# Performance work log

Measured on AMD Instinct MI355X. Metric: run time of the kernel, lower is better.

Reference implementation:

```python
import jax, jax.numpy as jnp
import numpy as np

N = 512      # N_res
C = 128      # act_dim == num_intermediate_channel
EPS = 1e-5   # torch LayerNorm default


def _layernorm(x, w, b):
    mu = jnp.mean(x, axis=-1, keepdims=True)
    var = jnp.var(x, axis=-1, keepdims=True)
    return (x - mu) * jax.lax.rsqrt(var + EPS) * w + b


def setup_inputs() -> dict:
    key = jax.random.key(0)
    ks = jax.random.split(key, 12)
    s_in = 1.0 / np.sqrt(C)
    inp = {
        "act": jax.random.normal(ks[0], (N, N, C), dtype=jnp.float32),
        "mask": jax.random.uniform(ks[1], (N, N), dtype=jnp.float32),
        # left_norm_input (LayerNorm over act_dim)
        "ln_in_w": jnp.ones((C,), jnp.float32),
        "ln_in_b": jnp.zeros((C,), jnp.float32),
        # projection: Linear(C -> 2C)
        "proj_w": jax.random.uniform(ks[2], (2 * C, C), jnp.float32, -s_in, s_in),
        "proj_b": jax.random.uniform(ks[3], (2 * C,), jnp.float32, -s_in, s_in),
        # gate: Linear(C -> 2C)
        "gate_w": jax.random.uniform(ks[4], (2 * C, C), jnp.float32, -s_in, s_in),
        "gate_b": jax.random.uniform(ks[5], (2 * C,), jnp.float32, -s_in, s_in),
        # center_norm (LayerNorm over num_intermediate_channel)
        "cn_w": jnp.ones((C,), jnp.float32),
        "cn_b": jnp.zeros((C,), jnp.float32),
        # output_projection: Linear(C -> C)
        "outp_w": jax.random.uniform(ks[6], (C, C), jnp.float32, -s_in, s_in),
        "outp_b": jax.random.uniform(ks[7], (C,), jnp.float32, -s_in, s_in),
        # gating_linear: Linear(C -> C)
        "gl_w": jax.random.uniform(ks[8], (C, C), jnp.float32, -s_in, s_in),
        "gl_b": jax.random.uniform(ks[9], (C,), jnp.float32, -s_in, s_in),
    }
    return inp


def reference(act, mask, ln_in_w, ln_in_b, proj_w, proj_b, gate_w, gate_b,
              cn_w, cn_b, outp_w, outp_b, gl_w, gl_b):
    m = mask[..., None]                                  # [N,N,1]
    x = _layernorm(act, ln_in_w, ln_in_b)                # [N,N,C]
    input_act = x
    proj = m * (jnp.einsum('ijc,dc->ijd', x, proj_w) + proj_b)      # [N,N,2C]
    proj = proj * jax.nn.sigmoid(jnp.einsum('ijc,dc->ijd', x, gate_w) + gate_b)
    left, right = proj[..., :C], proj[..., C:]           # each [N,N,C]
    # outgoing-edges triangular multiplication
    out = jnp.einsum('ikc,jkc->ijc', left, right)        # [N,N,C]
    out = _layernorm(out, cn_w, cn_b)
    out = jnp.einsum('ijc,dc->ijd', out, outp_w) + outp_b
    out = out * jax.nn.sigmoid(jnp.einsum('ijc,dc->ijd', input_act, gl_w) + gl_b)
    return out
```

## Files before the change

### kernel.cpp

```cpp
#include <hip/hip_runtime.h>
#include <hip/hip_bf16.h>


constexpr int TN = 512;
constexpr int TC = 128;
constexpr int TNP = TN * TN;
constexpr float TEPS = 1e-5f;

typedef __attribute__((ext_vector_type(8))) short s8b;
typedef __attribute__((ext_vector_type(4))) float f4;

__device__ __forceinline__ float wredsum(float v) {
#pragma unroll
    for (int off = 32; off > 0; off >>= 1) v += __shfl_xor(v, off);
    return v;
}
__device__ __forceinline__ float sigmoidf(float x) { return 1.0f / (1.0f + __expf(-x)); }
__device__ __forceinline__ unsigned short bfbits(float f) {
    __hip_bfloat16 h = __float2bfloat16(f);
    return *reinterpret_cast<unsigned short*>(&h);
}
__device__ __forceinline__ float bf2f(unsigned short u) {
    return __uint_as_float(((unsigned int)u) << 16);
}


extern "C" __global__ __launch_bounds__(256)
void k_wconv(const float* __restrict__ pw, const float* __restrict__ gw,
             const float* __restrict__ ow, const float* __restrict__ glw,
             const float* __restrict__ cnw,
             __hip_bfloat16* __restrict__ warr, __hip_bfloat16* __restrict__ wcat2)
{
    const int idx = blockIdx.x * 256 + threadIdx.x;
    if (idx < 65536) {
        const int j = idx & 7;
        const int slot = (idx >> 3) & 63;
        const int kg = (idx >> 9) & 3;
        const int rg = (idx >> 11) & 7;
        const int nc = idx >> 14;
        const int lh = slot & 15, lq = slot >> 4;
        const int row = rg * 16 + lh;
        const int k = kg * 32 + lq * 8 + j;
        const float v = (row < 64) ? pw[(nc * 64 + row) * TC + k]
                                   : gw[(nc * 64 + (row - 64)) * TC + k];
        warr[idx] = __float2bfloat16(v);
    } else if (idx < 98304) {
        const int j = idx - 65536;
        if (j < 16384) {
            const int c = j & 127;
            wcat2[j] = __float2bfloat16(cnw[c] * ow[j]);
        } else {
            wcat2[j] = __float2bfloat16(glw[j - 16384]);
        }
    }
}

extern "C" __global__ __launch_bounds__(128)
void k_sdt(const float* __restrict__ ow, const float* __restrict__ cnw,
           const float* __restrict__ cnb, const float* __restrict__ outp_b,
           float* __restrict__ Svec, float* __restrict__ Tbvec)
{
    const int d = threadIdx.x;
    float S = 0.f, T = 0.f;
    for (int c = 0; c < TC; ++c) {
        const float w = ow[d * TC + c];
        S += cnw[c] * w;
        T += cnb[c] * w;
    }
    Svec[d] = S;
    Tbvec[d] = T + outp_b[d];
}

extern "C" __global__ __launch_bounds__(256)
void k_ln(const float* __restrict__ act, const float* __restrict__ lnw,
          const float* __restrict__ lnb, __hip_bfloat16* __restrict__ xhp)
{
    __shared__ __align__(16) unsigned short t16[16 * 136];
    const int t = threadIdx.x, lane = t & 63, w = t >> 6;
    const int P0 = blockIdx.x * 64;
    const float2 wv = ((const float2*)lnw)[lane];
    const float2 bv = ((const float2*)lnb)[lane];
    unsigned short* xb = (unsigned short*)xhp;

    for (int r = 0; r < 4; ++r) {
#pragma unroll
        for (int q = 0; q < 4; ++q) {
            const int prow = w * 4 + q;
            const int p = P0 + r * 16 + prow;
            const float2 a = ((const float2*)(act + (size_t)p * TC))[lane];
            const float mu = wredsum(a.x + a.y) * (1.0f / 128.0f);
            const float d0 = a.x - mu, d1 = a.y - mu;
            const float var = wredsum(d0 * d0 + d1 * d1) * (1.0f / 128.0f);
            const float rs = rsqrtf(var + TEPS);
            ushort2 o;
            o.x = bfbits(d0 * rs * wv.x + bv.x);
            o.y = bfbits(d1 * rs * wv.y + bv.y);
            *(ushort2*)&t16[prow * 136 + lane * 2] = o;
        }
        __syncthreads();
        {
            const int kg = t >> 6, lq = (t >> 4) & 3, lh = t & 15;
            const s8b v = *(const s8b*)&t16[lh * 136 + kg * 32 + lq * 8];
            *(s8b*)(xb + (size_t)((P0 >> 4) + r) * 2048 + (size_t)t * 8) = v;
        }
        __syncthreads();
    }
}

extern "C" __global__ __launch_bounds__(256)
void k_proj(const __hip_bfloat16* __restrict__ xhp, const float* __restrict__ mask,
            const __hip_bfloat16* __restrict__ warr,
            const float* __restrict__ proj_b, const float* __restrict__ gate_b,
            __hip_bfloat16* __restrict__ lt, __hip_bfloat16* __restrict__ rt)
{
    __shared__ __align__(16) unsigned short Xls[128 * TC];
    __shared__ float msk[128];
    unsigned short* tls = Xls;

    const int t = threadIdx.x, lane = t & 63, w = t >> 6;
    const int lh = lane & 15, lq = lane >> 4;

    const int bid = blockIdx.x;
    const int work = (bid & 7) * 1024 + (bid >> 3);
    const int pt = work >> 2, dt = work & 3;
    const int P0 = pt * 128;

    const unsigned short* xb = (const unsigned short*)xhp;
    const unsigned short* wbc = (const unsigned short*)warr + (size_t)dt * 16384;

    if (t < 128) msk[t] = mask[P0 + t];

    const int wm = w >> 1, wn = w & 1;

#pragma unroll
    for (int s = 0; s < 8; ++s) {
        const int u = w * 8 + s;
        const size_t gu = ((size_t)(P0 >> 4) + (u >> 2)) * 4 + (u & 3);
        __builtin_amdgcn_global_load_lds(
            (const __attribute__((address_space(1))) unsigned*)(xb + gu * 512 + (size_t)lane * 8),
            (__attribute__((address_space(3))) unsigned*)&Xls[u * 512], 16, 0, 0);
    }

    s8b bc[4], bn[4];
#pragma unroll
    for (int nd = 0; nd < 2; ++nd) {
        bc[nd]     = *(const s8b*)(wbc + (size_t)(((wn * 2 + nd) * 4) + 0) * 512 + lane * 8);
        bc[2 + nd] = *(const s8b*)(wbc + (size_t)(((4 + wn * 2 + nd) * 4) + 0) * 512 + lane * 8);
    }
    __syncthreads();

    f4 acc[4][4];
#pragma unroll
    for (int mi = 0; mi < 4; ++mi)
#pragma unroll
        for (int ni = 0; ni < 4; ++ni)
            acc[mi][ni] = (f4){0.f, 0.f, 0.f, 0.f};

#pragma unroll
    for (int kg = 0; kg < 4; ++kg) {
        if (kg < 3) {
#pragma unroll
            for (int nd = 0; nd < 2; ++nd) {
                bn[nd]     = *(const s8b*)(wbc + (size_t)(((wn * 2 + nd) * 4) + kg + 1) * 512 + lane * 8);
                bn[2 + nd] = *(const s8b*)(wbc + (size_t)(((4 + wn * 2 + nd) * 4) + kg + 1) * 512 + lane * 8);
            }
        }
        s8b af[4];
#pragma unroll
        for (int mi = 0; mi < 4; ++mi)
            af[mi] = *(const s8b*)&Xls[(((wm * 4 + mi) * 4) + kg) * 512 + lane * 8];
#pragma unroll
        for (int mi = 0; mi < 4; ++mi)
#pragma unroll
            for (int ni = 0; ni < 4; ++ni)
                acc[mi][ni] = __builtin_amdgcn_mfma_f32_16x16x32_bf16(
                    af[mi], bc[ni], acc[mi][ni], 0, 0, 0);
        if (kg < 3) {
#pragma unroll
            for (int ni = 0; ni < 4; ++ni) bc[ni] = bn[ni];
        }
    }
    __syncthreads();

#pragma unroll
    for (int mi = 0; mi < 4; ++mi)
#pragma unroll
        for (int nd = 0; nd < 2; ++nd) {
            const int dl = wn * 32 + nd * 16 + lh;
            const float pbv = proj_b[dt * 64 + dl];
            const float gbv = gate_b[dt * 64 + dl];
            const f4 P = acc[mi][nd];
            const f4 G = acc[mi][2 + nd];
            const int pbase = wm * 64 + mi * 16 + lq * 4;
            float v[4];
#pragma unroll
            for (int r = 0; r < 4; ++r)
                v[r] = msk[pbase + r] * (P[r] + pbv) * sigmoidf(G[r] + gbv);
            ushort2 u01, u23;
            u01.x = bfbits(v[0]); u01.y = bfbits(v[1]);
            u23.x = bfbits(v[2]); u23.y = bfbits(v[3]);
            *(ushort2*)&tls[dl * 134 + pbase]     = u01;
            *(ushort2*)&tls[dl * 134 + pbase + 2] = u23;
        }
    __syncthreads();

    {
        __hip_bfloat16* dst0 = (dt < 2) ? lt + (size_t)(dt * 64) * TNP
                                        : rt + (size_t)((dt - 2) * 64) * TNP;
#pragma unroll
        for (int rr = 0; rr < 16; ++rr) {
            const int dl = w * 16 + rr;
            const ushort2 v = *(const ushort2*)&tls[dl * 134 + lane * 2];
            *(ushort2*)((unsigned short*)(dst0 + (size_t)dl * TNP) + P0 + lane * 2) = v;
        }
    }
}

extern "C" __global__ __launch_bounds__(256)
void k_tri_mfma(const __hip_bfloat16* __restrict__ lt,
                const __hip_bfloat16* __restrict__ rt,
                __hip_bfloat16* __restrict__ trih)
{
    __shared__ __align__(16) char smem[128 * 136 * 2];
    __hip_bfloat16* Als = (__hip_bfloat16*)smem;
    __hip_bfloat16* Bls = (__hip_bfloat16*)(smem + 8192);
    unsigned short* Cls = (unsigned short*)smem;

    const int bid = blockIdx.x;
    const int work = (bid & 7) * 256 + (bid >> 3);
    const int c = work >> 4, tt = work & 15;
    const int i0 = (tt >> 2) * 128, j0 = (tt & 3) * 128;

    const int t = threadIdx.x;
    const int w = t >> 6, lane = t & 63;
    const int wm = w >> 1, wn = w & 1;
    const int lh = lane & 15, lq = lane >> 4;

    const size_t cbase = (size_t)c * TNP;
    const int srow = lane >> 2;
    const int scol = (lane & 3) * 8;

    f4 acc[4][4];
#pragma unroll
    for (int mi = 0; mi < 4; ++mi)
#pragma unroll
        for (int ni = 0; ni < 4; ++ni)
            acc[mi][ni] = (f4){0.f, 0.f, 0.f, 0.f};

    for (int k0 = 0; k0 < TN; k0 += 32) {
        __syncthreads();
#pragma unroll
        for (int s = 0; s < 2; ++s) {
            const int r0 = w * 32 + s * 16;
            const __hip_bfloat16* ga = lt + cbase + (size_t)(i0 + r0 + srow) * TN + k0 + scol;
            const __hip_bfloat16* gb = rt + cbase + (size_t)(j0 + r0 + srow) * TN + k0 + scol;
            __builtin_amdgcn_global_load_lds(
                (const __attribute__((address_space(1))) unsigned*)ga,
                (__attribute__((address_space(3))) unsigned*)&Als[r0 * 32], 16, 0, 0);
            __builtin_amdgcn_global_load_lds(
                (const __attribute__((address_space(1))) unsigned*)gb,
                (__attribute__((address_space(3))) unsigned*)&Bls[r0 * 32], 16, 0, 0);
        }
        __syncthreads();

        s8b afr[4], bfr[4];
#pragma unroll
        for (int mi = 0; mi < 4; ++mi)
            afr[mi] = *(const s8b*)&Als[(wm * 64 + mi * 16 + lh) * 32 + lq * 8];
#pragma unroll
        for (int ni = 0; ni < 4; ++ni)
            bfr[ni] = *(const s8b*)&Bls[(wn * 64 + ni * 16 + lh) * 32 + lq * 8];
#pragma unroll
        for (int mi = 0; mi < 4; ++mi)
#pragma unroll
            for (int ni = 0; ni < 4; ++ni)
                acc[mi][ni] = __builtin_amdgcn_mfma_f32_16x16x32_bf16(
                    afr[mi], bfr[ni], acc[mi][ni], 0, 0, 0);
    }

    __syncthreads();
#pragma unroll
    for (int mi = 0; mi < 4; ++mi)
#pragma unroll
        for (int ni = 0; ni < 4; ++ni) {
            const f4 v = acc[mi][ni];
            const int jl = wn * 64 + ni * 16 + lh;
#pragma unroll
            for (int r = 0; r < 4; ++r) {
                const int il = wm * 64 + mi * 16 + lq * 4 + r;
                Cls[il * 136 + jl] = bfbits(v[r]);
            }
        }
    __syncthreads();
    {
        unsigned short* ob = (unsigned short*)trih + cbase;
#pragma unroll
        for (int qq = 0; qq < 8; ++qq) {
            const int row = qq * 16 + (t >> 4);
            const int c16 = t & 15;
            const s8b v = *(const s8b*)&Cls[row * 136 + c16 * 8];
            *(s8b*)&ob[(size_t)(i0 + row) * TN + j0 + c16 * 8] = v;
        }
    }
}

constexpr int PB = 64;

extern "C" __global__ __launch_bounds__(256)
void k_out_proj(const __hip_bfloat16* __restrict__ trih,
                const __hip_bfloat16* __restrict__ xhp,
                const __hip_bfloat16* __restrict__ wcat2,
                const float* __restrict__ Svec, const float* __restrict__ Tbvec,
                const float* __restrict__ gl_b,
                float* __restrict__ outb)
{
    __shared__ __align__(16) unsigned short yfr[PB * TC];
    __shared__ float2 sred[4][PB];
    __shared__ float2 stats[PB];

    const int t = threadIdx.x, lane = t & 63, w = t >> 6;
    const int lh = lane & 15, lq = lane >> 4;
    const int P0 = blockIdx.x * PB;
    const unsigned short* tb = (const unsigned short*)trih;
    const unsigned short* xb = (const unsigned short*)xhp;
    const unsigned short* wb = (const unsigned short*)wcat2;

    {
        const int p = lane;
        const int ub = (p >> 4) * 4 + w;
        const int sl = p & 15;
        float s = 0.f, s2 = 0.f;
#pragma unroll
        for (int q = 0; q < 4; ++q) {
            unsigned short tmp[8];
#pragma unroll
            for (int j = 0; j < 8; ++j) {
                const int c = w * 32 + q * 8 + j;
                tmp[j] = tb[(size_t)c * TNP + P0 + p];
                const float f = bf2f(tmp[j]);
                s += f; s2 += f * f;
            }
            *(s8b*)&yfr[ub * 512 + (q * 16 + sl) * 8] = *(const s8b*)tmp;
        }
        sred[w][p] = make_float2(s, s2);
    }
    __syncthreads();
    if (t < PB) {
        float s = 0.f, s2 = 0.f;
#pragma unroll
        for (int g = 0; g < 4; ++g) {
            const float2 v = sred[g][t];
            s += v.x; s2 += v.y;
        }
        const float mu = s * (1.0f / 128.0f);
        const float var = s2 * (1.0f / 128.0f) - mu * mu;
        stats[t] = make_float2(mu, rsqrtf(var + TEPS));
    }
    __syncthreads();

    const int dO = w * 32;
    const int dG = 128 + w * 32;

    f4 acc[4][4];
#pragma unroll
    for (int mi = 0; mi < 4; ++mi)
#pragma unroll
        for (int ni = 0; ni < 4; ++ni)
            acc[mi][ni] = (f4){0.f, 0.f, 0.f, 0.f};

#pragma unroll
    for (int kg = 0; kg < 4; ++kg) {
        s8b bo[2], bg[2], ay[4], ah[4];
#pragma unroll
        for (int nd = 0; nd < 2; ++nd) {
            bo[nd] = *(const s8b*)(wb + (dO + nd * 16 + lh) * TC + kg * 32 + lq * 8);
            bg[nd] = *(const s8b*)(wb + (dG + nd * 16 + lh) * TC + kg * 32 + lq * 8);
        }
#pragma unroll
        for (int mi = 0; mi < 4; ++mi) {
            ay[mi] = *(const s8b*)&yfr[(mi * 4 + kg) * 512 + lane * 8];
            ah[mi] = *(const s8b*)(xb + (size_t)((P0 >> 4) + mi) * 2048
                                      + kg * 512 + (size_t)lane * 8);
        }
#pragma unroll
        for (int mi = 0; mi < 4; ++mi)
#pragma unroll
            for (int nd = 0; nd < 2; ++nd) {
                acc[mi][nd]     = __builtin_amdgcn_mfma_f32_16x16x32_bf16(
                    ay[mi], bo[nd], acc[mi][nd], 0, 0, 0);
                acc[mi][2 + nd] = __builtin_amdgcn_mfma_f32_16x16x32_bf16(
                    ah[mi], bg[nd], acc[mi][2 + nd], 0, 0, 0);
            }
    }

    float Sd[2], Tbd[2], glb[2];
#pragma unroll
    for (int nd = 0; nd < 2; ++nd) {
        const int d = w * 32 + nd * 16 + lh;
        Sd[nd]  = Svec[d];
        Tbd[nd] = Tbvec[d];
        glb[nd] = gl_b[d];
    }
#pragma unroll
    for (int mi = 0; mi < 4; ++mi)
#pragma unroll
        for (int nd = 0; nd < 2; ++nd) {
            const f4 G = acc[mi][nd];
            const f4 Gg = acc[mi][2 + nd];
            const int d = w * 32 + nd * 16 + lh;
#pragma unroll
            for (int r = 0; r < 4; ++r) {
                const int ploc = mi * 16 + lq * 4 + r;
                const float2 st = stats[ploc];
                const float o = st.y * G[r] - st.y * st.x * Sd[nd] + Tbd[nd];
                outb[(size_t)(P0 + ploc) * TC + d] = o * sigmoidf(Gg[r] + glb[nd]);
            }
        }
}

extern "C" void kernel_launch(void* const* d_in, const int* in_sizes, int n_in,
                              void* d_out, int out_size, void* d_ws, size_t ws_size,
                              hipStream_t stream)
{
    const float* act    = (const float*)d_in[0];
    const float* mask   = (const float*)d_in[1];
    const float* lnw    = (const float*)d_in[2];
    const float* lnb    = (const float*)d_in[3];
    const float* proj_w = (const float*)d_in[4];
    const float* proj_b = (const float*)d_in[5];
    const float* gate_w = (const float*)d_in[6];
    const float* gate_b = (const float*)d_in[7];
    const float* cnw    = (const float*)d_in[8];
    const float* cnb    = (const float*)d_in[9];
    const float* outp_w = (const float*)d_in[10];
    const float* outp_b = (const float*)d_in[11];
    const float* gl_w   = (const float*)d_in[12];
    const float* gl_b   = (const float*)d_in[13];

    __hip_bfloat16* lt   = (__hip_bfloat16*)d_ws;
    __hip_bfloat16* rt   = lt + (size_t)TC * TNP;
    __hip_bfloat16* xhp  = rt + (size_t)TC * TNP;
    __hip_bfloat16* trih = xhp + (size_t)TNP * TC;
    __hip_bfloat16* warr = trih + (size_t)TC * TNP;
    __hip_bfloat16* wcat2 = warr + 4 * 128 * TC;
    float* Svec  = (float*)(wcat2 + 2 * TC * TC);
    float* Tbvec = Svec + TC;
    float* out = (float*)d_out;

    k_wconv<<<384, 256, 0, stream>>>(proj_w, gate_w, outp_w, gl_w, cnw, warr, wcat2);
    k_sdt<<<1, 128, 0, stream>>>(outp_w, cnw, cnb, outp_b, Svec, Tbvec);
    k_ln<<<TNP / 64, 256, 0, stream>>>(act, lnw, lnb, xhp);
    k_proj<<<8192, 256, 0, stream>>>(xhp, mask, warr, proj_b, gate_b, lt, rt);
    k_tri_mfma<<<2048, 256, 0, stream>>>(lt, rt, trih);
    k_out_proj<<<TNP / PB, 256, 0, stream>>>(trih, xhp, wcat2, Svec, Tbvec,
                                             gl_b, out);
}
```

Before: 282.2 us.

## Fuse gating-linear GEMM into projection kernel and store sigmoid gate as bf16

The gating_linear weights are packed into the projection weight array, so k_proj runs a fifth MFMA column tile per k-step and writes sigmoid(x·Wg + b) as a bf16 [N,N,C] buffer. k_out_proj then only runs the output-projection GEMM and multiplies by the loaded gate, no longer rereading the normalized input or doing the second GEMM. The triangular output buffer now aliases the no-longer-needed normalized-input buffer to keep the workspace small. In exchange, k_proj gains extra registers and accumulators and drops its weight prefetch double-buffering, the 32 MB gate tensor must be written and read back, and the gate is rounded to bf16.

```diff
diff --git a/kernel.cpp b/kernel.cpp
--- a/kernel.cpp
+++ b/kernel.cpp
@@ -32,26 +32,25 @@
              __hip_bfloat16* __restrict__ warr, __hip_bfloat16* __restrict__ wcat2)
 {
     const int idx = blockIdx.x * 256 + threadIdx.x;
-    if (idx < 65536) {
-        const int j = idx & 7;
-        const int slot = (idx >> 3) & 63;
-        const int kg = (idx >> 9) & 3;
-        const int rg = (idx >> 11) & 7;
-        const int nc = idx >> 14;
+    if (idx < 81920) {
+        const int nc = idx / 20480;
+        const int rem = idx % 20480;
+        const int unit = rem >> 9;
+        const int rg = unit >> 2, kg = unit & 3;
+        const int off = rem & 511;
+        const int slot = off >> 3, j = off & 7;
         const int lh = slot & 15, lq = slot >> 4;
         const int row = rg * 16 + lh;
         const int k = kg * 32 + lq * 8 + j;
-        const float v = (row < 64) ? pw[(nc * 64 + row) * TC + k]
-                                   : gw[(nc * 64 + (row - 64)) * TC + k];
+        float v;
+        if (row < 64)       v = pw[(nc * 64 + row) * TC + k];
+        else if (row < 128) v = gw[(nc * 64 + (row - 64)) * TC + k];
+        else                v = glw[(nc * 32 + (row - 128)) * TC + k];
         warr[idx] = __float2bfloat16(v);
-    } else if (idx < 98304) {
-        const int j = idx - 65536;
-        if (j < 16384) {
-            const int c = j & 127;
-            wcat2[j] = __float2bfloat16(cnw[c] * ow[j]);
-        } else {
-            wcat2[j] = __float2bfloat16(glw[j - 16384]);
-        }
+    } else {
+        const int j2 = idx - 81920;
+        const int c = j2 & 127;
+        wcat2[j2] = __float2bfloat16(cnw[c] * ow[j2]);
     }
 }
 
@@ -111,7 +110,9 @@
 void k_proj(const __hip_bfloat16* __restrict__ xhp, const float* __restrict__ mask,
             const __hip_bfloat16* __restrict__ warr,
             const float* __restrict__ proj_b, const float* __restrict__ gate_b,
-            __hip_bfloat16* __restrict__ lt, __hip_bfloat16* __restrict__ rt)
+            const float* __restrict__ gl_b,
+            __hip_bfloat16* __restrict__ lt, __hip_bfloat16* __restrict__ rt,
+            __hip_bfloat16* __restrict__ glgb)
 {
     __shared__ __align__(16) unsigned short Xls[128 * TC];
     __shared__ float msk[128];
@@ -126,7 +127,8 @@
     const int P0 = pt * 128;
 
     const unsigned short* xb = (const unsigned short*)xhp;
-    const unsigned short* wbc = (const unsigned short*)warr + (size_t)dt * 16384;
+    const unsigned short* wbc = (const unsigned short*)warr + (size_t)dt * 20480;
+    unsigned short* gb = (unsigned short*)glgb;
 
     if (t < 128) msk[t] = mask[P0 + t];
 
@@ -140,47 +142,48 @@
             (const __attribute__((address_space(1))) unsigned*)(xb + gu * 512 + (size_t)lane * 8),
             (__attribute__((address_space(3))) unsigned*)&Xls[u * 512], 16, 0, 0);
     }
-
-    s8b bc[4], bn[4];
-#pragma unroll
-    for (int nd = 0; nd < 2; ++nd) {
-        bc[nd]     = *(const s8b*)(wbc + (size_t)(((wn * 2 + nd) * 4) + 0) * 512 + lane * 8);
-        bc[2 + nd] = *(const s8b*)(wbc + (size_t)(((4 + wn * 2 + nd) * 4) + 0) * 512 + lane * 8);
-    }
-    __syncthreads();
-
-    f4 acc[4][4];
-#pragma unroll
-    for (int mi = 0; mi < 4; ++mi)
-#pragma unroll
-        for (int ni = 0; ni < 4; ++ni)
+    __syncthreads();
+
+    f4 acc[4][5];
+#pragma unroll
+    for (int mi = 0; mi < 4; ++mi)
+#pragma unroll
+        for (int ni = 0; ni < 5; ++ni)
             acc[mi][ni] = (f4){0.f, 0.f, 0.f, 0.f};
 
 #pragma unroll
     for (int kg = 0; kg < 4; ++kg) {
-        if (kg < 3) {
-#pragma unroll
-            for (int nd = 0; nd < 2; ++nd) {
-                bn[nd]     = *(const s8b*)(wbc + (size_t)(((wn * 2 + nd) * 4) + kg + 1) * 512 + lane * 8);
-                bn[2 + nd] = *(const s8b*)(wbc + (size_t)(((4 + wn * 2 + nd) * 4) + kg + 1) * 512 + lane * 8);
-            }
-        }
-        s8b af[4];
+        s8b bfr[5], af[4];
+#pragma unroll
+        for (int nd = 0; nd < 2; ++nd) {
+            bfr[nd]     = *(const s8b*)(wbc + (size_t)(((wn * 2 + nd) * 4) + kg) * 512 + lane * 8);
+            bfr[2 + nd] = *(const s8b*)(wbc + (size_t)((((4 + wn * 2 + nd)) * 4) + kg) * 512 + lane * 8);
+        }
+        bfr[4] = *(const s8b*)(wbc + (size_t)(((8 + wn) * 4) + kg) * 512 + lane * 8);
 #pragma unroll
         for (int mi = 0; mi < 4; ++mi)
             af[mi] = *(const s8b*)&Xls[(((wm * 4 + mi) * 4) + kg) * 512 + lane * 8];
 #pragma unroll
         for (int mi = 0; mi < 4; ++mi)
 #pragma unroll
-            for (int ni = 0; ni < 4; ++ni)
+            for (int ni = 0; ni < 5; ++ni)
                 acc[mi][ni] = __builtin_amdgcn_mfma_f32_16x16x32_bf16(
-                    af[mi], bc[ni], acc[mi][ni], 0, 0, 0);
-        if (kg < 3) {
-#pragma unroll
-            for (int ni = 0; ni < 4; ++ni) bc[ni] = bn[ni];
-        }
-    }
-    __syncthreads();
+                    af[mi], bfr[ni], acc[mi][ni], 0, 0, 0);
+    }
+    __syncthreads();
+
+    {
+        const float glbv = gl_b[dt * 32 + wn * 16 + lh];
+#pragma unroll
+        for (int mi = 0; mi < 4; ++mi) {
+            const f4 Gl = acc[mi][4];
+            const int pbase = wm * 64 + mi * 16 + lq * 4;
+#pragma unroll
+            for (int r = 0; r < 4; ++r)
+                gb[(size_t)(P0 + pbase + r) * TC + dt * 32 + wn * 16 + lh] =
+                    bfbits(sigmoidf(Gl[r] + glbv));
+        }
+    }
 
 #pragma unroll
     for (int mi = 0; mi < 4; ++mi)
@@ -253,12 +256,12 @@
         for (int s = 0; s < 2; ++s) {
             const int r0 = w * 32 + s * 16;
             const __hip_bfloat16* ga = lt + cbase + (size_t)(i0 + r0 + srow) * TN + k0 + scol;
-            const __hip_bfloat16* gb = rt + cbase + (size_t)(j0 + r0 + srow) * TN + k0 + scol;
+            const __hip_bfloat16* gbp = rt + cbase + (size_t)(j0 + r0 + srow) * TN + k0 + scol;
             __builtin_amdgcn_global_load_lds(
                 (const __attribute__((address_space(1))) unsigned*)ga,
                 (__attribute__((address_space(3))) unsigned*)&Als[r0 * 32], 16, 0, 0);
             __builtin_amdgcn_global_load_lds(
-                (const __attribute__((address_space(1))) unsigned*)gb,
+                (const __attribute__((address_space(1))) unsigned*)gbp,
                 (__attribute__((address_space(3))) unsigned*)&Bls[r0 * 32], 16, 0, 0);
         }
         __syncthreads();
@@ -308,10 +311,9 @@
 
 extern "C" __global__ __launch_bounds__(256)
 void k_out_proj(const __hip_bfloat16* __restrict__ trih,
-                const __hip_bfloat16* __restrict__ xhp,
+                const __hip_bfloat16* __restrict__ glgb,
                 const __hip_bfloat16* __restrict__ wcat2,
                 const float* __restrict__ Svec, const float* __restrict__ Tbvec,
-                const float* __restrict__ gl_b,
                 float* __restrict__ outb)
 {
     __shared__ __align__(16) unsigned short yfr[PB * TC];
@@ -322,7 +324,7 @@
     const int lh = lane & 15, lq = lane >> 4;
     const int P0 = blockIdx.x * PB;
     const unsigned short* tb = (const unsigned short*)trih;
-    const unsigned short* xb = (const unsigned short*)xhp;
+    const unsigned short* gb = (const unsigned short*)glgb;
     const unsigned short* wb = (const unsigned short*)wcat2;
 
     {
@@ -359,61 +361,51 @@
     __syncthreads();
 
     const int dO = w * 32;
-    const int dG = 128 + w * 32;
-
-    f4 acc[4][4];
-#pragma unroll
-    for (int mi = 0; mi < 4; ++mi)
-#pragma unroll
-        for (int ni = 0; ni < 4; ++ni)
+
+    f4 acc[4][2];
+#pragma unroll
+    for (int mi = 0; mi < 4; ++mi)
+#pragma unroll
+        for (int ni = 0; ni < 2; ++ni)
             acc[mi][ni] = (f4){0.f, 0.f, 0.f, 0.f};
 
 #pragma unroll
     for (int kg = 0; kg < 4; ++kg) {
-        s8b bo[2], bg[2], ay[4], ah[4];
-#pragma unroll
-        for (int nd = 0; nd < 2; ++nd) {
+        s8b bo[2], ay[4];
+#pragma unroll
+        for (int nd = 0; nd < 2; ++nd)
             bo[nd] = *(const s8b*)(wb + (dO + nd * 16 + lh) * TC + kg * 32 + lq * 8);
-            bg[nd] = *(const s8b*)(wb + (dG + nd * 16 + lh) * TC + kg * 32 + lq * 8);
-        }
-#pragma unroll
-        for (int mi = 0; mi < 4; ++mi) {
+#pragma unroll
+        for (int mi = 0; mi < 4; ++mi)
             ay[mi] = *(const s8b*)&yfr[(mi * 4 + kg) * 512 + lane * 8];
-            ah[mi] = *(const s8b*)(xb + (size_t)((P0 >> 4) + mi) * 2048
-                                      + kg * 512 + (size_t)lane * 8);
-        }
-#pragma unroll
-        for (int mi = 0; mi < 4; ++mi)
-#pragma unroll
-            for (int nd = 0; nd < 2; ++nd) {
-                acc[mi][nd]     = __builtin_amdgcn_mfma_f32_16x16x32_bf16(
+#pragma unroll
+        for (int mi = 0; mi < 4; ++mi)
+#pragma unroll
+            for (int nd = 0; nd < 2; ++nd)
+                acc[mi][nd] = __builtin_amdgcn_mfma_f32_16x16x32_bf16(
                     ay[mi], bo[nd], acc[mi][nd], 0, 0, 0);
-                acc[mi][2 + nd] = __builtin_amdgcn_mfma_f32_16x16x32_bf16(
-                    ah[mi], bg[nd], acc[mi][2 + nd], 0, 0, 0);
-            }
-    }
-
-    float Sd[2], Tbd[2], glb[2];
+    }
+
+    float Sd[2], Tbd[2];
 #pragma unroll
     for (int nd = 0; nd < 2; ++nd) {
         const int d = w * 32 + nd * 16 + lh;
         Sd[nd]  = Svec[d];
         Tbd[nd] = Tbvec[d];
-        glb[nd] = gl_b[d];
     }
 #pragma unroll
     for (int mi = 0; mi < 4; ++mi)
 #pragma unroll
         for (int nd = 0; nd < 2; ++nd) {
             const f4 G = acc[mi][nd];
-            const f4 Gg = acc[mi][2 + nd];
             const int d = w * 32 + nd * 16 + lh;
 #pragma unroll
             for (int r = 0; r < 4; ++r) {
                 const int ploc = mi * 16 + lq * 4 + r;
                 const float2 st = stats[ploc];
                 const float o = st.y * G[r] - st.y * st.x * Sd[nd] + Tbd[nd];
-                outb[(size_t)(P0 + ploc) * TC + d] = o * sigmoidf(Gg[r] + glb[nd]);
+                const float g = bf2f(gb[(size_t)(P0 + ploc) * TC + d]);
+                outb[(size_t)(P0 + ploc) * TC + d] = o * g;
             }
         }
 }
@@ -440,18 +432,19 @@
     __hip_bfloat16* lt   = (__hip_bfloat16*)d_ws;
     __hip_bfloat16* rt   = lt + (size_t)TC * TNP;
     __hip_bfloat16* xhp  = rt + (size_t)TC * TNP;
-    __hip_bfloat16* trih = xhp + (size_t)TNP * TC;
-    __hip_bfloat16* warr = trih + (size_t)TC * TNP;
-    __hip_bfloat16* wcat2 = warr + 4 * 128 * TC;
-    float* Svec  = (float*)(wcat2 + 2 * TC * TC);
+    __hip_bfloat16* trih = xhp;
+    __hip_bfloat16* glgb = xhp + (size_t)TNP * TC;
+    __hip_bfloat16* warr = glgb + (size_t)TNP * TC;
+    __hip_bfloat16* wcat2 = warr + 81920;
+    float* Svec  = (float*)(wcat2 + 16384);
     float* Tbvec = Svec + TC;
     float* out = (float*)d_out;
 
     k_wconv<<<384, 256, 0, stream>>>(proj_w, gate_w, outp_w, gl_w, cnw, warr, wcat2);
     k_sdt<<<1, 128, 0, stream>>>(outp_w, cnw, cnb, outp_b, Svec, Tbvec);
     k_ln<<<TNP / 64, 256, 0, stream>>>(act, lnw, lnb, xhp);
-    k_proj<<<8192, 256, 0, stream>>>(xhp, mask, warr, proj_b, gate_b, lt, rt);
+    k_proj<<<8192, 256, 0, stream>>>(xhp, mask, warr, proj_b, gate_b, gl_b,
+                                     lt, rt, glgb);
     k_tri_mfma<<<2048, 256, 0, stream>>>(lt, rt, trih);
-    k_out_proj<<<TNP / PB, 256, 0, stream>>>(trih, xhp, wcat2, Svec, Tbvec,
-                                             gl_b, out);
-}
+    k_out_proj<<<TNP / PB, 256, 0, stream>>>(trih, glgb, wcat2, Svec, Tbvec, out);
+}
```

Result: slower. 295.8 us (+4.8%).

## Restructure output projection into single-wave blocks over 16 positions and half the channels

Applied to the files above, without the earlier changes.

The output-projection kernel now runs one 64-thread wave per block, covering 16 positions and 64 output channels, instead of 256 threads covering 64 positions. LayerNorm statistics are reduced with wave shuffles instead of shared-memory reductions and block barriers. The goal is more, smaller blocks with no block-level syncs, for better latency hiding and occupancy. In exchange, each 16-position tile of the triangular-multiply output is read and normalised twice (once per channel half), and there are many more tiny blocks to schedule.

```diff
diff --git a/kernel.cpp b/kernel.cpp
--- a/kernel.cpp
+++ b/kernel.cpp
@@ -253,12 +253,12 @@
         for (int s = 0; s < 2; ++s) {
             const int r0 = w * 32 + s * 16;
             const __hip_bfloat16* ga = lt + cbase + (size_t)(i0 + r0 + srow) * TN + k0 + scol;
-            const __hip_bfloat16* gb = rt + cbase + (size_t)(j0 + r0 + srow) * TN + k0 + scol;
+            const __hip_bfloat16* gbp = rt + cbase + (size_t)(j0 + r0 + srow) * TN + k0 + scol;
             __builtin_amdgcn_global_load_lds(
                 (const __attribute__((address_space(1))) unsigned*)ga,
                 (__attribute__((address_space(3))) unsigned*)&Als[r0 * 32], 16, 0, 0);
             __builtin_amdgcn_global_load_lds(
-                (const __attribute__((address_space(1))) unsigned*)gb,
+                (const __attribute__((address_space(1))) unsigned*)gbp,
                 (__attribute__((address_space(3))) unsigned*)&Bls[r0 * 32], 16, 0, 0);
         }
         __syncthreads();
@@ -304,9 +304,7 @@
     }
 }
 
-constexpr int PB = 64;
-
-extern "C" __global__ __launch_bounds__(256)
+extern "C" __global__ __launch_bounds__(64)
 void k_out_proj(const __hip_bfloat16* __restrict__ trih,
                 const __hip_bfloat16* __restrict__ xhp,
                 const __hip_bfloat16* __restrict__ wcat2,
@@ -314,108 +312,77 @@
                 const float* __restrict__ gl_b,
                 float* __restrict__ outb)
 {
-    __shared__ __align__(16) unsigned short yfr[PB * TC];
-    __shared__ float2 sred[4][PB];
-    __shared__ float2 stats[PB];
-
-    const int t = threadIdx.x, lane = t & 63, w = t >> 6;
+    __shared__ __align__(16) unsigned short yfr[4 * 512];
+
+    const int lane = threadIdx.x;
     const int lh = lane & 15, lq = lane >> 4;
-    const int P0 = blockIdx.x * PB;
+    const int bid = blockIdx.x;
+    const int g = bid >> 1;
+    const int D0 = (bid & 1) * 64;
+    const int P0 = g * 16;
     const unsigned short* tb = (const unsigned short*)trih;
     const unsigned short* xb = (const unsigned short*)xhp;
     const unsigned short* wb = (const unsigned short*)wcat2;
 
-    {
-        const int p = lane;
-        const int ub = (p >> 4) * 4 + w;
-        const int sl = p & 15;
-        float s = 0.f, s2 = 0.f;
-#pragma unroll
-        for (int q = 0; q < 4; ++q) {
-            unsigned short tmp[8];
-#pragma unroll
-            for (int j = 0; j < 8; ++j) {
-                const int c = w * 32 + q * 8 + j;
-                tmp[j] = tb[(size_t)c * TNP + P0 + p];
-                const float f = bf2f(tmp[j]);
-                s += f; s2 += f * f;
-            }
-            *(s8b*)&yfr[ub * 512 + (q * 16 + sl) * 8] = *(const s8b*)tmp;
-        }
-        sred[w][p] = make_float2(s, s2);
-    }
-    __syncthreads();
-    if (t < PB) {
-        float s = 0.f, s2 = 0.f;
-#pragma unroll
-        for (int g = 0; g < 4; ++g) {
-            const float2 v = sred[g][t];
-            s += v.x; s2 += v.y;
-        }
-        const float mu = s * (1.0f / 128.0f);
-        const float var = s2 * (1.0f / 128.0f) - mu * mu;
-        stats[t] = make_float2(mu, rsqrtf(var + TEPS));
-    }
-    __syncthreads();
-
-    const int dO = w * 32;
-    const int dG = 128 + w * 32;
-
-    f4 acc[4][4];
-#pragma unroll
-    for (int mi = 0; mi < 4; ++mi)
-#pragma unroll
-        for (int ni = 0; ni < 4; ++ni)
-            acc[mi][ni] = (f4){0.f, 0.f, 0.f, 0.f};
-
+    float s = 0.f, s2 = 0.f;
 #pragma unroll
     for (int kg = 0; kg < 4; ++kg) {
-        s8b bo[2], bg[2], ay[4], ah[4];
-#pragma unroll
-        for (int nd = 0; nd < 2; ++nd) {
-            bo[nd] = *(const s8b*)(wb + (dO + nd * 16 + lh) * TC + kg * 32 + lq * 8);
-            bg[nd] = *(const s8b*)(wb + (dG + nd * 16 + lh) * TC + kg * 32 + lq * 8);
-        }
-#pragma unroll
-        for (int mi = 0; mi < 4; ++mi) {
-            ay[mi] = *(const s8b*)&yfr[(mi * 4 + kg) * 512 + lane * 8];
-            ah[mi] = *(const s8b*)(xb + (size_t)((P0 >> 4) + mi) * 2048
-                                      + kg * 512 + (size_t)lane * 8);
-        }
-#pragma unroll
-        for (int mi = 0; mi < 4; ++mi)
-#pragma unroll
-            for (int nd = 0; nd < 2; ++nd) {
-                acc[mi][nd]     = __builtin_amdgcn_mfma_f32_16x16x32_bf16(
-                    ay[mi], bo[nd], acc[mi][nd], 0, 0, 0);
-                acc[mi][2 + nd] = __builtin_amdgcn_mfma_f32_16x16x32_bf16(
-                    ah[mi], bg[nd], acc[mi][2 + nd], 0, 0, 0);
-            }
-    }
-
-    float Sd[2], Tbd[2], glb[2];
-#pragma unroll
-    for (int nd = 0; nd < 2; ++nd) {
-        const int d = w * 32 + nd * 16 + lh;
-        Sd[nd]  = Svec[d];
-        Tbd[nd] = Tbvec[d];
-        glb[nd] = gl_b[d];
-    }
-#pragma unroll
-    for (int mi = 0; mi < 4; ++mi)
-#pragma unroll
-        for (int nd = 0; nd < 2; ++nd) {
-            const f4 G = acc[mi][nd];
-            const f4 Gg = acc[mi][2 + nd];
-            const int d = w * 32 + nd * 16 + lh;
-#pragma unroll
-            for (int r = 0; r < 4; ++r) {
-                const int ploc = mi * 16 + lq * 4 + r;
-                const float2 st = stats[ploc];
-                const float o = st.y * G[r] - st.y * st.x * Sd[nd] + Tbd[nd];
-                outb[(size_t)(P0 + ploc) * TC + d] = o * sigmoidf(Gg[r] + glb[nd]);
-            }
-        }
+        unsigned short tmp[8];
+#pragma unroll
+        for (int j = 0; j < 8; ++j) {
+            const int c = kg * 32 + lq * 8 + j;
+            tmp[j] = tb[(size_t)c * TNP + P0 + lh];
+            const float f = bf2f(tmp[j]);
+            s += f; s2 += f * f;
+        }
+        *(s8b*)&yfr[kg * 512 + lane * 8] = *(const s8b*)tmp;
+    }
+    s  += __shfl_xor(s, 16);  s  += __shfl_xor(s, 32);
+    s2 += __shfl_xor(s2, 16); s2 += __shfl_xor(s2, 32);
+    const float mu = s * (1.0f / 128.0f);
+    const float var = s2 * (1.0f / 128.0f) - mu * mu;
+    const float rs = rsqrtf(var + TEPS);
+    __builtin_amdgcn_wave_barrier();
+
+    f4 acc[8];
+#pragma unroll
+    for (int i = 0; i < 8; ++i) acc[i] = (f4){0.f, 0.f, 0.f, 0.f};
+
+#pragma unroll
+    for (int kg = 0; kg < 4; ++kg) {
+        const s8b ay = *(const s8b*)&yfr[kg * 512 + lane * 8];
+        const s8b ah = *(const s8b*)(xb + (size_t)g * 2048 + kg * 512 + (size_t)lane * 8);
+#pragma unroll
+        for (int nd = 0; nd < 4; ++nd) {
+            const int d = D0 + nd * 16 + lh;
+            const s8b bo = *(const s8b*)(wb + (size_t)d * TC + kg * 32 + lq * 8);
+            const s8b bg = *(const s8b*)(wb + (size_t)(128 + d) * TC + kg * 32 + lq * 8);
+            acc[nd]     = __builtin_amdgcn_mfma_f32_16x16x32_bf16(ay, bo, acc[nd], 0, 0, 0);
+            acc[4 + nd] = __builtin_amdgcn_mfma_f32_16x16x32_bf16(ah, bg, acc[4 + nd], 0, 0, 0);
+        }
+    }
+
+    float mus[4], rss[4];
+#pragma unroll
+    for (int r = 0; r < 4; ++r) {
+        mus[r] = __shfl(mu, lq * 4 + r);
+        rss[r] = __shfl(rs, lq * 4 + r);
+    }
+
+#pragma unroll
+    for (int nd = 0; nd < 4; ++nd) {
+        const int d = D0 + nd * 16 + lh;
+        const float Sd  = Svec[d];
+        const float Tbd = Tbvec[d];
+        const float glb = gl_b[d];
+        const f4 G  = acc[nd];
+        const f4 Gl = acc[4 + nd];
+#pragma unroll
+        for (int r = 0; r < 4; ++r) {
+            const float o = rss[r] * G[r] - rss[r] * mus[r] * Sd + Tbd;
+            outb[(size_t)(P0 + lq * 4 + r) * TC + d] = o * sigmoidf(Gl[r] + glb);
+        }
+    }
 }
 
 extern "C" void kernel_launch(void* const* d_in, const int* in_sizes, int n_in,
@@ -452,6 +419,6 @@
     k_ln<<<TNP / 64, 256, 0, stream>>>(act, lnw, lnb, xhp);
     k_proj<<<8192, 256, 0, stream>>>(xhp, mask, warr, proj_b, gate_b, lt, rt);
     k_tri_mfma<<<2048, 256, 0, stream>>>(lt, rt, trih);
-    k_out_proj<<<TNP / PB, 256, 0, stream>>>(trih, xhp, wcat2, Svec, Tbvec,
-                                             gl_b, out);
-}
+    k_out_proj<<<TNP / 16 * 2, 64, 0, stream>>>(trih, xhp, wcat2, Svec, Tbvec,
+                                                gl_b, out);
+}
```

Result: slower. 364.3 us (+29.1%).

## Enlarge out-projection tile and stage output through LDS for coalesced stores

Applied to the files above, without the earlier changes.

The output-projection kernel now handles 128 positions per block with 512 threads instead of 64 positions with 256. Each thread reads two adjacent positions per channel as ushort2 when loading the channel-major triangle result. Work is split across a 4x2 wave grid. The final fp32 output is written into a reused LDS tile in two passes and then stored as float4 rows, replacing scattered scalar stores. This targets poor coalescing on both the transposed input reads and the output writes, at the cost of more LDS traffic and extra barriers.

```diff
diff --git a/kernel.cpp b/kernel.cpp
--- a/kernel.cpp
+++ b/kernel.cpp
@@ -253,12 +253,12 @@
         for (int s = 0; s < 2; ++s) {
             const int r0 = w * 32 + s * 16;
             const __hip_bfloat16* ga = lt + cbase + (size_t)(i0 + r0 + srow) * TN + k0 + scol;
-            const __hip_bfloat16* gb = rt + cbase + (size_t)(j0 + r0 + srow) * TN + k0 + scol;
+            const __hip_bfloat16* gbp = rt + cbase + (size_t)(j0 + r0 + srow) * TN + k0 + scol;
             __builtin_amdgcn_global_load_lds(
                 (const __attribute__((address_space(1))) unsigned*)ga,
                 (__attribute__((address_space(3))) unsigned*)&Als[r0 * 32], 16, 0, 0);
             __builtin_amdgcn_global_load_lds(
-                (const __attribute__((address_space(1))) unsigned*)gb,
+                (const __attribute__((address_space(1))) unsigned*)gbp,
                 (__attribute__((address_space(3))) unsigned*)&Bls[r0 * 32], 16, 0, 0);
         }
         __syncthreads();
@@ -304,9 +304,7 @@
     }
 }
 
-constexpr int PB = 64;
-
-extern "C" __global__ __launch_bounds__(256)
+extern "C" __global__ __launch_bounds__(512)
 void k_out_proj(const __hip_bfloat16* __restrict__ trih,
                 const __hip_bfloat16* __restrict__ xhp,
                 const __hip_bfloat16* __restrict__ wcat2,
@@ -314,42 +312,49 @@
                 const float* __restrict__ gl_b,
                 float* __restrict__ outb)
 {
-    __shared__ __align__(16) unsigned short yfr[PB * TC];
-    __shared__ float2 sred[4][PB];
-    __shared__ float2 stats[PB];
+    __shared__ __align__(16) char smem[41984];
+    unsigned short* yfr = (unsigned short*)smem;
+    float2* sred = (float2*)(smem + 32768);
+    float2* stats = (float2*)(smem + 40960);
+    float* otile = (float*)smem;
 
     const int t = threadIdx.x, lane = t & 63, w = t >> 6;
     const int lh = lane & 15, lq = lane >> 4;
-    const int P0 = blockIdx.x * PB;
+    const int P0 = blockIdx.x * 128;
     const unsigned short* tb = (const unsigned short*)trih;
     const unsigned short* xb = (const unsigned short*)xhp;
     const unsigned short* wb = (const unsigned short*)wcat2;
 
     {
-        const int p = lane;
-        const int ub = (p >> 4) * 4 + w;
-        const int sl = p & 15;
+        const int p0 = 2 * lane, p1 = 2 * lane + 1;
+        float s0 = 0.f, s20 = 0.f, s1 = 0.f, s21 = 0.f;
+#pragma unroll
+        for (int q = 0; q < 2; ++q) {
+            unsigned short t0[8], t1[8];
+#pragma unroll
+            for (int j = 0; j < 8; ++j) {
+                const int c = w * 16 + q * 8 + j;
+                const ushort2 v = *(const ushort2*)(tb + (size_t)c * TNP + P0 + p0);
+                t0[j] = v.x; t1[j] = v.y;
+                const float f0 = bf2f(v.x), f1 = bf2f(v.y);
+                s0 += f0; s20 += f0 * f0;
+                s1 += f1; s21 += f1 * f1;
+            }
+            const int cb = w * 16 + q * 8;
+            const int kg = cb >> 5, sq = (cb >> 3) & 3;
+            const int u = (p0 >> 4) * 4 + kg;
+            *(s8b*)&yfr[u * 512 + (sq * 16 + (p0 & 15)) * 8] = *(const s8b*)t0;
+            *(s8b*)&yfr[u * 512 + (sq * 16 + (p1 & 15)) * 8] = *(const s8b*)t1;
+        }
+        sred[w * 128 + p0] = make_float2(s0, s20);
+        sred[w * 128 + p1] = make_float2(s1, s21);
+    }
+    __syncthreads();
+    if (t < 128) {
         float s = 0.f, s2 = 0.f;
 #pragma unroll
-        for (int q = 0; q < 4; ++q) {
-            unsigned short tmp[8];
-#pragma unroll
-            for (int j = 0; j < 8; ++j) {
-                const int c = w * 32 + q * 8 + j;
-                tmp[j] = tb[(size_t)c * TNP + P0 + p];
-                const float f = bf2f(tmp[j]);
-                s += f; s2 += f * f;
-            }
-            *(s8b*)&yfr[ub * 512 + (q * 16 + sl) * 8] = *(const s8b*)tmp;
-        }
-        sred[w][p] = make_float2(s, s2);
-    }
-    __syncthreads();
-    if (t < PB) {
-        float s = 0.f, s2 = 0.f;
-#pragma unroll
-        for (int g = 0; g < 4; ++g) {
-            const float2 v = sred[g][t];
+        for (int g = 0; g < 8; ++g) {
+            const float2 v = sred[g * 128 + t];
             s += v.x; s2 += v.y;
         }
         const float mu = s * (1.0f / 128.0f);
@@ -358,64 +363,88 @@
     }
     __syncthreads();
 
-    const int dO = w * 32;
-    const int dG = 128 + w * 32;
-
-    f4 acc[4][4];
-#pragma unroll
-    for (int mi = 0; mi < 4; ++mi)
-#pragma unroll
-        for (int ni = 0; ni < 4; ++ni)
+    const int wm = w >> 1, wn = w & 1;
+
+    f4 acc[2][8];
+#pragma unroll
+    for (int mi = 0; mi < 2; ++mi)
+#pragma unroll
+        for (int ni = 0; ni < 8; ++ni)
             acc[mi][ni] = (f4){0.f, 0.f, 0.f, 0.f};
 
 #pragma unroll
     for (int kg = 0; kg < 4; ++kg) {
-        s8b bo[2], bg[2], ay[4], ah[4];
-#pragma unroll
-        for (int nd = 0; nd < 2; ++nd) {
-            bo[nd] = *(const s8b*)(wb + (dO + nd * 16 + lh) * TC + kg * 32 + lq * 8);
-            bg[nd] = *(const s8b*)(wb + (dG + nd * 16 + lh) * TC + kg * 32 + lq * 8);
-        }
-#pragma unroll
-        for (int mi = 0; mi < 4; ++mi) {
-            ay[mi] = *(const s8b*)&yfr[(mi * 4 + kg) * 512 + lane * 8];
-            ah[mi] = *(const s8b*)(xb + (size_t)((P0 >> 4) + mi) * 2048
+        s8b bo[4], bg[4], ay[2], ah[2];
+#pragma unroll
+        for (int nd = 0; nd < 4; ++nd) {
+            const int d = wn * 64 + nd * 16 + lh;
+            bo[nd] = *(const s8b*)(wb + (size_t)d * TC + kg * 32 + lq * 8);
+            bg[nd] = *(const s8b*)(wb + (size_t)(128 + d) * TC + kg * 32 + lq * 8);
+        }
+#pragma unroll
+        for (int mi = 0; mi < 2; ++mi) {
+            const int g = wm * 2 + mi;
+            ay[mi] = *(const s8b*)&yfr[(g * 4 + kg) * 512 + lane * 8];
+            ah[mi] = *(const s8b*)(xb + ((size_t)(P0 >> 4) + g) * 2048
                                       + kg * 512 + (size_t)lane * 8);
         }
 #pragma unroll
-        for (int mi = 0; mi < 4; ++mi)
-#pragma unroll
-            for (int nd = 0; nd < 2; ++nd) {
+        for (int mi = 0; mi < 2; ++mi)
+#pragma unroll
+            for (int nd = 0; nd < 4; ++nd) {
                 acc[mi][nd]     = __builtin_amdgcn_mfma_f32_16x16x32_bf16(
                     ay[mi], bo[nd], acc[mi][nd], 0, 0, 0);
-                acc[mi][2 + nd] = __builtin_amdgcn_mfma_f32_16x16x32_bf16(
-                    ah[mi], bg[nd], acc[mi][2 + nd], 0, 0, 0);
+                acc[mi][4 + nd] = __builtin_amdgcn_mfma_f32_16x16x32_bf16(
+                    ah[mi], bg[nd], acc[mi][4 + nd], 0, 0, 0);
             }
     }
 
-    float Sd[2], Tbd[2], glb[2];
-#pragma unroll
-    for (int nd = 0; nd < 2; ++nd) {
-        const int d = w * 32 + nd * 16 + lh;
+    float Sd[4], Tbd[4], glb[4];
+#pragma unroll
+    for (int nd = 0; nd < 4; ++nd) {
+        const int d = wn * 64 + nd * 16 + lh;
         Sd[nd]  = Svec[d];
         Tbd[nd] = Tbvec[d];
         glb[nd] = gl_b[d];
     }
-#pragma unroll
-    for (int mi = 0; mi < 4; ++mi)
-#pragma unroll
-        for (int nd = 0; nd < 2; ++nd) {
-            const f4 G = acc[mi][nd];
-            const f4 Gg = acc[mi][2 + nd];
-            const int d = w * 32 + nd * 16 + lh;
-#pragma unroll
-            for (int r = 0; r < 4; ++r) {
-                const int ploc = mi * 16 + lq * 4 + r;
-                const float2 st = stats[ploc];
-                const float o = st.y * G[r] - st.y * st.x * Sd[nd] + Tbd[nd];
-                outb[(size_t)(P0 + ploc) * TC + d] = o * sigmoidf(Gg[r] + glb[nd]);
-            }
-        }
+    float mus[2][4], rss[2][4];
+#pragma unroll
+    for (int mi = 0; mi < 2; ++mi)
+#pragma unroll
+        for (int r = 0; r < 4; ++r) {
+            const float2 st = stats[wm * 32 + mi * 16 + lq * 4 + r];
+            mus[mi][r] = st.x; rss[mi][r] = st.y;
+        }
+
+#pragma unroll
+    for (int pass = 0; pass < 2; ++pass) {
+        __syncthreads();
+        if ((wm >> 1) == pass) {
+#pragma unroll
+            for (int mi = 0; mi < 2; ++mi)
+#pragma unroll
+                for (int nd = 0; nd < 4; ++nd) {
+                    const f4 G  = acc[mi][nd];
+                    const f4 Gl = acc[mi][4 + nd];
+                    const int col = wn * 64 + nd * 16 + lh;
+#pragma unroll
+                    for (int r = 0; r < 4; ++r) {
+                        const int row = (wm & 1) * 32 + mi * 16 + lq * 4 + r;
+                        const float o = rss[mi][r] * G[r]
+                                      - rss[mi][r] * mus[mi][r] * Sd[nd] + Tbd[nd];
+                        otile[row * 132 + col] = o * sigmoidf(Gl[r] + glb[nd]);
+                    }
+                }
+        }
+        __syncthreads();
+#pragma unroll
+        for (int it = 0; it < 4; ++it) {
+            const int i = it * 512 + t;
+            const int row = i >> 5, c16 = i & 31;
+            const float4 v = *(const float4*)&otile[row * 132 + c16 * 4];
+            *(float4*)&outb[(size_t)(P0 + pass * 64 + row) * TC + c16 * 4] = v;
+        }
+    }
 }
 
 extern "C" void kernel_launch(void* const* d_in, const int* in_sizes, int n_in,
@@ -452,6 +481,6 @@
     k_ln<<<TNP / 64, 256, 0, stream>>>(act, lnw, lnb, xhp);
     k_proj<<<8192, 256, 0, stream>>>(xhp, mask, warr, proj_b, gate_b, lt, rt);
     k_tri_mfma<<<2048, 256, 0, stream>>>(lt, rt, trih);
-    k_out_proj<<<TNP / PB, 256, 0, stream>>>(trih, xhp, wcat2, Svec, Tbvec,
-                                             gl_b, out);
-}
+    k_out_proj<<<TNP / 128, 512, 0, stream>>>(trih, xhp, wcat2, Svec, Tbvec,
+                                              gl_b, out);
+}
```

Result: slower. 307.6 us (+9.0%).
